# Optimization experiments

Hardware: AMD Instinct MI355X
Metric: run time of the kernel (lower is better)

Reference implementation:

```python
import jax, jax.numpy as jnp
import numpy as np

D_MODEL = 1024
N_HEADS = 16
D_HEAD = D_MODEL // N_HEADS


def setup_inputs() -> dict:
    key = jax.random.key(0)
    k_x, k_wqkv, k_bqkv, k_wo, k_bo = jax.random.split(key, 5)
    B, S = 2, 2048
    x = jax.random.normal(k_x, (B, S, D_MODEL), dtype=jnp.float32)
    # torch Linear: y = x @ W.T + b; store W as [out, in] like torch
    bound1 = 1.0 / np.sqrt(D_MODEL)
    W_qkv = jax.random.uniform(k_wqkv, (3 * D_MODEL, D_MODEL), minval=-bound1, maxval=bound1, dtype=jnp.float32)
    b_qkv = jax.random.uniform(k_bqkv, (3 * D_MODEL,), minval=-bound1, maxval=bound1, dtype=jnp.float32)
    W_out = jax.random.uniform(k_wo, (D_MODEL, D_MODEL), minval=-bound1, maxval=bound1, dtype=jnp.float32)
    b_out = jax.random.uniform(k_bo, (D_MODEL,), minval=-bound1, maxval=bound1, dtype=jnp.float32)
    return {"x": x, "W_qkv": W_qkv, "b_qkv": b_qkv, "W_out": W_out, "b_out": b_out}


def reference(x, W_qkv, b_qkv, W_out, b_out):
    B, S, D = x.shape
    qkv = x @ W_qkv.T + b_qkv                       # [B, S, 3D]
    qkv = qkv.reshape(B, S, 3, N_HEADS, D_HEAD)
    qkv = jnp.transpose(qkv, (2, 0, 3, 1, 4))       # [3, B, H, S, Dh]
    q, k, v = qkv[0], qkv[1], qkv[2]
    scores = jnp.einsum('bhqd,bhkd->bhqk', q, k) / np.sqrt(D_HEAD).astype(np.float32)
    causal = jnp.tril(jnp.ones((S, S), dtype=bool))
    scores = jnp.where(causal[None, None], scores, jnp.float32(-jnp.inf))
    attn = jax.nn.softmax(scores, axis=-1)          # dropout p=0 -> identity
    out = jnp.einsum('bhqk,bhkd->bhqd', attn, v)    # [B, H, S, Dh]
    out = jnp.transpose(out, (0, 2, 1, 3)).reshape(B, S, D)
    return out @ W_out.T + b_out
```

## Files before the change

### kernel.cpp

```cpp
#include <hip/hip_runtime.h>
#include <hip/hip_bf16.h>
#include <cstdint>


#define DEV __device__ __forceinline__

#define VT_STRIDE 2048

using bf16x8 = __attribute__((ext_vector_type(8))) short;
using f32x4  = __attribute__((ext_vector_type(4))) float;

DEV unsigned short f2bf(float f) {
  unsigned u = __builtin_bit_cast(unsigned, f);
  u = (u + 0x7fffu + ((u >> 16) & 1u)) >> 16;
  return (unsigned short)u;
}

typedef __attribute__((address_space(1))) unsigned int as1_uint;
typedef __attribute__((address_space(3))) unsigned int as3_uint;

DEV void gload_lds16(const void* g, void* l) {
  __builtin_amdgcn_global_load_lds(
      (as1_uint*)(uintptr_t)g,
      (as3_uint*)(unsigned int)(uintptr_t)l,
      16, 0, 0);
}

#define N4_X  (4096 * 1024 / 4)
#define N4_WQ (3072 * 1024 / 4)
#define N4_WO (1024 * 1024 / 4)
__global__ __launch_bounds__(256) void cvt_all_k(const float* __restrict__ x,
                                                 const float* __restrict__ wq,
                                                 const float* __restrict__ wo,
                                                 unsigned short* __restrict__ xb,
                                                 unsigned short* __restrict__ wqb,
                                                 unsigned short* __restrict__ wob) {
  int i = blockIdx.x * 256 + threadIdx.x;
  const float* in; unsigned short* out;
  if (i < N4_X)                { in = x;  out = xb; }
  else if (i < N4_X + N4_WQ)   { i -= N4_X;  in = wq; out = wqb; }
  else                         { i -= N4_X + N4_WQ; in = wo; out = wob; }
  float4 v = reinterpret_cast<const float4*>(in)[i];
  ushort4 o;
  o.x = f2bf(v.x); o.y = f2bf(v.y); o.z = f2bf(v.z); o.w = f2bf(v.w);
  reinterpret_cast<ushort4*>(out)[i] = o;
}

__global__ __launch_bounds__(256) void transpose_v_k(const unsigned short* __restrict__ V,
                                                     unsigned short* __restrict__ Vt) {
  const int bh = blockIdx.x;
  const int st = blockIdx.y;
  const int tid = threadIdx.x;
  __shared__ unsigned short T[64 * 64];
  const unsigned short* src = V + ((size_t)bh * 2048 + st * 64) * 64;

#pragma unroll
  for (int it = 0; it < 2; ++it) {
    const int c = it * 256 + tid;
    const int L = c * 16;
    const int S = L ^ (((L >> 10) & 7) << 4);
    gload_lds16((const char*)src + S, (char*)T + L);
  }
  __syncthreads();

#pragma unroll
  for (int it = 0; it < 2; ++it) {
    const int c = it * 256 + tid;
    const int d = c >> 3;
    const int s_off = (c & 7) * 8;
    const int xg = (c & 7) << 4;
    bf16x8 pk;
#pragma unroll
    for (int j = 0; j < 8; ++j)
      pk[j] = *(const short*)((const char*)T + (((s_off + j) * 128 + d * 2) ^ xg));
    *(bf16x8*)(Vt + (size_t)(bh * 64 + d) * VT_STRIDE + st * 64 + s_off) = pk;
  }
}

template <int MODE, int N, int K>
__global__ __launch_bounds__(256) void gemm_bt(const unsigned short* __restrict__ A,
                                               const unsigned short* __restrict__ W,
                                               const float* __restrict__ bias,
                                               float* __restrict__ Cout,
                                               unsigned short* __restrict__ Qp,
                                               unsigned short* __restrict__ Kp,
                                               unsigned short* __restrict__ Vp) {
  __shared__ unsigned short As[128 * 64];
  __shared__ unsigned short Bs[128 * 64];
  const int tid = threadIdx.x;
  const int m0 = blockIdx.x * 128;
  const int n0 = blockIdx.y * 128;
  const int w = tid >> 6, lane = tid & 63, g = lane >> 4, lr = lane & 15;
  const int wr = w >> 1, wc = w & 1;
  const int xr = (lr & 7) << 4;

  f32x4 acc[4][4];
#pragma unroll
  for (int i = 0; i < 4; ++i)
#pragma unroll
    for (int j = 0; j < 4; ++j)
#pragma unroll
      for (int r = 0; r < 4; ++r) acc[i][j][r] = 0.f;

  for (int kt = 0; kt < K; kt += 64) {
#pragma unroll
    for (int it = 0; it < 4; ++it) {
      const int c = it * 256 + tid;
      const int row = c >> 3;
      const int colb = ((c & 7) * 16) ^ ((row & 7) << 4);
      gload_lds16((const char*)(A + (size_t)(m0 + row) * K + kt) + colb, (char*)As + c * 16);
      gload_lds16((const char*)(W + (size_t)(n0 + row) * K + kt) + colb, (char*)Bs + c * 16);
    }
    __syncthreads();
#pragma unroll
    for (int ks = 0; ks < 2; ++ks) {
      bf16x8 af[4], bf[4];
#pragma unroll
      for (int mi = 0; mi < 4; ++mi)
        af[mi] = *(const bf16x8*)((const char*)As +
                   ((((wr * 64 + mi * 16 + lr) * 128) + ks * 64 + g * 16) ^ xr));
#pragma unroll
      for (int ni = 0; ni < 4; ++ni)
        bf[ni] = *(const bf16x8*)((const char*)Bs +
                   ((((wc * 64 + ni * 16 + lr) * 128) + ks * 64 + g * 16) ^ xr));
#pragma unroll
      for (int mi = 0; mi < 4; ++mi)
#pragma unroll
        for (int ni = 0; ni < 4; ++ni)
          acc[mi][ni] = __builtin_amdgcn_mfma_f32_16x16x32_bf16(af[mi], bf[ni], acc[mi][ni], 0, 0, 0);
    }
    __syncthreads();
  }

  if (MODE == 0) {
#pragma unroll
    for (int ni = 0; ni < 4; ++ni) {
      const int col = n0 + wc * 64 + ni * 16 + lr;
      const float bv = bias[col];
#pragma unroll
      for (int mi = 0; mi < 4; ++mi)
#pragma unroll
        for (int r = 0; r < 4; ++r) {
          const int row = m0 + wr * 64 + mi * 16 + g * 4 + r;
          Cout[(size_t)row * N + col] = acc[mi][ni][r] + bv;
        }
    }
  } else {
#pragma unroll
    for (int ni = 0; ni < 4; ++ni) {
      const int col = n0 + wc * 64 + ni * 16 + lr;
      const float bv = bias[col];
      const int which = col >> 10;
      const int h = (col >> 6) & 15;
      const int d = col & 63;
      unsigned short* P = which == 0 ? Qp : which == 1 ? Kp : Vp;
#pragma unroll
      for (int mi = 0; mi < 4; ++mi)
#pragma unroll
        for (int r = 0; r < 4; ++r) {
          const int row = m0 + wr * 64 + mi * 16 + g * 4 + r;
          const int b = row >> 11, s = row & 2047;
          P[(((size_t)(b * 16 + h) * 2048 + s) << 6) + d] = f2bf(acc[mi][ni][r] + bv);
        }
    }
  }
}

__global__ __launch_bounds__(256) void attn_fwd(const unsigned short* __restrict__ Q,
                                                const unsigned short* __restrict__ Kg,
                                                const unsigned short* __restrict__ Vt,
                                                unsigned short* __restrict__ AO) {
  const int bh = blockIdx.x;
  const int qb = blockIdx.y;
  const int tid = threadIdx.x;
  const int w = tid >> 6, lane = tid & 63, g = lane >> 4, lr = lane & 15;
  const unsigned short* Qp = Q  + (size_t)bh * 2048 * 64;
  const unsigned short* Kp = Kg + (size_t)bh * 2048 * 64;
  const unsigned short* Vp = Vt + (size_t)bh * 64 * VT_STRIDE;
  const int b = bh >> 4, h = bh & 15;

  __shared__ unsigned short Ks[2][64 * 64];
  __shared__ unsigned short Vs[2][64 * 64];
  __shared__ unsigned short Pl[4][16 * 64];

  const float C = 0.1803368801f;
  char* Plw = (char*)Pl[w];
  const int xr = (lr & 7) << 4;

  const int L0 = tid * 16,         L1 = (tid + 256) * 16;
  const int G0 = L0 ^ (((L0 >> 7) & 7) << 4);
  const int G1 = L1 ^ (((L1 >> 7) & 7) << 4);

#define STAGE(buf, kvb)                                                                     \
  do {                                                                                      \
    gload_lds16((const char*)Kp + (size_t)(kvb) * 128 + G0, (char*)Ks[buf] + L0);           \
    gload_lds16((const char*)Kp + (size_t)(kvb) * 128 + G1, (char*)Ks[buf] + L1);           \
    gload_lds16((const char*)Vp + (size_t)(G0 >> 7) * (VT_STRIDE * 2) + (size_t)(kvb) * 2 + \
                    (G0 & 127), (char*)Vs[buf] + L0);                                       \
    gload_lds16((const char*)Vp + (size_t)(G1 >> 7) * (VT_STRIDE * 2) + (size_t)(kvb) * 2 + \
                    (G1 & 127), (char*)Vs[buf] + L1);                                       \
  } while (0)

#pragma unroll
  for (int half = 0; half < 2; ++half) {
    const int qt = half ? (31 - qb) : qb;
    const int nb = qt + 1;
    const int qrow0 = qt * 64 + w * 16;

    bf16x8 aq[2];
#pragma unroll
    for (int ks = 0; ks < 2; ++ks)
      aq[ks] = *(const bf16x8*)(Qp + (size_t)(qrow0 + lr) * 64 + ks * 32 + g * 8);

    f32x4 o[4];
    float lp = 0.f;
#pragma unroll
    for (int db = 0; db < 4; ++db)
#pragma unroll
      for (int r = 0; r < 4; ++r) o[db][r] = 0.f;

    STAGE(0, 0);
    int cur = 0;

    for (int t = 0; t < nb; ++t) {
      if (t + 1 < nb) {
        STAGE(cur ^ 1, (t + 1) * 64);
        asm volatile("s_waitcnt vmcnt(4)" ::: "memory");
      } else {
        asm volatile("s_waitcnt vmcnt(0)" ::: "memory");
      }
      __builtin_amdgcn_s_barrier();
      __builtin_amdgcn_sched_barrier(0);

      const char* KsC = (const char*)Ks[cur];
      const char* VsC = (const char*)Vs[cur];

      f32x4 sc[4];
#pragma unroll
      for (int f = 0; f < 4; ++f)
#pragma unroll
        for (int r = 0; r < 4; ++r) sc[f][r] = 0.f;
      __builtin_amdgcn_s_setprio(1);
#pragma unroll
      for (int ks = 0; ks < 2; ++ks)
#pragma unroll
        for (int f = 0; f < 4; ++f) {
          bf16x8 bk = *(const bf16x8*)(KsC + (((f * 16 + lr) * 128 + ks * 64 + g * 16) ^ xr));
          sc[f] = __builtin_amdgcn_mfma_f32_16x16x32_bf16(bk, aq[ks], sc[f], 0, 0, 0);
        }
      __builtin_amdgcn_s_setprio(0);

      if (t == nb - 1) {
        const int thr = w * 16 + lr - g * 4;
#pragma unroll
        for (int f = 0; f < 4; ++f)
#pragma unroll
          for (int r = 0; r < 4; ++r)
            if (f * 16 + r > thr) sc[f][r] = -INFINITY;
      }

#pragma unroll
      for (int f = 0; f < 4; ++f) {
        float p0 = exp2f(sc[f][0] * C);
        float p1 = exp2f(sc[f][1] * C);
        float p2 = exp2f(sc[f][2] * C);
        float p3 = exp2f(sc[f][3] * C);
        sc[f][0] = p0; sc[f][1] = p1; sc[f][2] = p2; sc[f][3] = p3;
        lp += (p0 + p1) + (p2 + p3);
      }

#pragma unroll
      for (int f = 0; f < 4; ++f) {
        unsigned w0, w1;
        asm("v_cvt_pk_bf16_f32 %0, %1, %2" : "=v"(w0) : "v"(sc[f][0]), "v"(sc[f][1]));
        asm("v_cvt_pk_bf16_f32 %0, %1, %2" : "=v"(w1) : "v"(sc[f][2]), "v"(sc[f][3]));
        uint2 pk; pk.x = w0; pk.y = w1;
        *(uint2*)(Plw + ((lr * 128 + f * 32 + g * 8) ^ xr)) = pk;
      }
      asm volatile("s_waitcnt lgkmcnt(0)" ::: "memory");
      __builtin_amdgcn_sched_barrier(0);

      __builtin_amdgcn_s_setprio(1);
#pragma unroll
      for (int ks = 0; ks < 2; ++ks) {
        bf16x8 pa = *(const bf16x8*)(Plw + ((lr * 128 + ks * 64 + g * 16) ^ xr));
#pragma unroll
        for (int db = 0; db < 4; ++db) {
          bf16x8 bv = *(const bf16x8*)(VsC + (((db * 16 + lr) * 128 + ks * 64 + g * 16) ^ xr));
          o[db] = __builtin_amdgcn_mfma_f32_16x16x32_bf16(pa, bv, o[db], 0, 0, 0);
        }
      }
      __builtin_amdgcn_s_setprio(0);

      asm volatile("" ::: "memory");
      __builtin_amdgcn_s_barrier();
      __builtin_amdgcn_sched_barrier(0);
      cur ^= 1;
    }

    lp += __shfl_xor(lp, 16);
    lp += __shfl_xor(lp, 32);
    const float inv = 1.0f / lp;
#pragma unroll
    for (int r = 0; r < 4; ++r) {
      const float linv = __shfl(inv, g * 4 + r);
      const int row = qrow0 + g * 4 + r;
#pragma unroll
      for (int db = 0; db < 4; ++db)
        AO[(size_t)(b * 2048 + row) * 1024 + h * 64 + db * 16 + lr] = f2bf(o[db][r] * linv);
    }
  }
#undef STAGE
}

extern "C" void kernel_launch(void* const* d_in, const int* in_sizes, int n_in,
                              void* d_out, int out_size, void* d_ws, size_t ws_size,
                              hipStream_t stream) {
  const float* x     = (const float*)d_in[0];
  const float* W_qkv = (const float*)d_in[1];
  const float* b_qkv = (const float*)d_in[2];
  const float* W_out = (const float*)d_in[3];
  const float* b_out = (const float*)d_in[4];
  float* out = (float*)d_out;

  char* ws = (char*)d_ws;
  unsigned short* xb  = (unsigned short*)(ws);
  unsigned short* AOb = (unsigned short*)(ws);
  unsigned short* wqb = (unsigned short*)(ws + ((size_t)8 << 20));
  unsigned short* wob = (unsigned short*)(ws + ((size_t)14 << 20));
  unsigned short* Qb  = (unsigned short*)(ws + ((size_t)16 << 20));
  unsigned short* Kb  = (unsigned short*)(ws + ((size_t)24 << 20));
  unsigned short* Vb  = (unsigned short*)(ws + ((size_t)32 << 20));
  unsigned short* Vtb = (unsigned short*)(ws + ((size_t)40 << 20));

  cvt_all_k<<<(N4_X + N4_WQ + N4_WO) / 256, 256, 0, stream>>>(x, W_qkv, W_out, xb, wqb, wob);

  gemm_bt<1, 3072, 1024><<<dim3(32, 24), 256, 0, stream>>>(xb, wqb, b_qkv, nullptr, Qb, Kb, Vb);
  transpose_v_k<<<dim3(32, 32), 256, 0, stream>>>(Vb, Vtb);
  attn_fwd<<<dim3(32, 16), 256, 0, stream>>>(Qb, Kb, Vtb, AOb);
  gemm_bt<0, 1024, 1024><<<dim3(32, 8), 256, 0, stream>>>(AOb, wob, b_out, out, nullptr, nullptr, nullptr);
}
```

Baseline: 124.0 us.

## Double-buffer GEMM LDS tiles to overlap global loads with MFMA

Converts the bf16 GEMM main loop to a two-stage LDS ping-pong: the next K-tile is issued via global_load_lds while the current tile is consumed by MFMAs, with manual vmcnt waits and raw barriers. It also raises wave priority around the MFMA section. This targets exposed global-load latency between K steps, at the cost of doubling LDS use (64KB per block), which may cut occupancy.

```diff
diff --git a/kernel.cpp b/kernel.cpp
--- a/kernel.cpp
+++ b/kernel.cpp
@@ -85,8 +85,8 @@
                                                unsigned short* __restrict__ Qp,
                                                unsigned short* __restrict__ Kp,
                                                unsigned short* __restrict__ Vp) {
-  __shared__ unsigned short As[128 * 64];
-  __shared__ unsigned short Bs[128 * 64];
+  __shared__ unsigned short As[2][128 * 64];
+  __shared__ unsigned short Bs[2][128 * 64];
   const int tid = threadIdx.x;
   const int m0 = blockIdx.x * 128;
   const int n0 = blockIdx.y * 128;
@@ -102,26 +102,46 @@
 #pragma unroll
       for (int r = 0; r < 4; ++r) acc[i][j][r] = 0.f;
 
-  for (int kt = 0; kt < K; kt += 64) {
-#pragma unroll
-    for (int it = 0; it < 4; ++it) {
-      const int c = it * 256 + tid;
-      const int row = c >> 3;
-      const int colb = ((c & 7) * 16) ^ ((row & 7) << 4);
-      gload_lds16((const char*)(A + (size_t)(m0 + row) * K + kt) + colb, (char*)As + c * 16);
-      gload_lds16((const char*)(W + (size_t)(n0 + row) * K + kt) + colb, (char*)Bs + c * 16);
-    }
-    __syncthreads();
+#define GSTAGE(buf, kt)                                                                     \
+  do {                                                                                      \
+    _Pragma("unroll")                                                                       \
+    for (int it = 0; it < 4; ++it) {                                                        \
+      const int c = it * 256 + tid;                                                         \
+      const int row = c >> 3;                                                               \
+      const int colb = ((c & 7) * 16) ^ ((row & 7) << 4);                                   \
+      gload_lds16((const char*)(A + (size_t)(m0 + row) * K + (kt)) + colb,                  \
+                  (char*)As[buf] + c * 16);                                                 \
+      gload_lds16((const char*)(W + (size_t)(n0 + row) * K + (kt)) + colb,                  \
+                  (char*)Bs[buf] + c * 16);                                                 \
+    }                                                                                       \
+  } while (0)
+
+  GSTAGE(0, 0);
+  int cur = 0;
+  const int nsteps = K / 64;
+  for (int step = 0; step < nsteps; ++step) {
+    if (step + 1 < nsteps) {
+      GSTAGE(cur ^ 1, (step + 1) * 64);
+      asm volatile("s_waitcnt vmcnt(8)" ::: "memory");
+    } else {
+      asm volatile("s_waitcnt vmcnt(0)" ::: "memory");
+    }
+    __builtin_amdgcn_s_barrier();
+    __builtin_amdgcn_sched_barrier(0);
+
+    const char* AsC = (const char*)As[cur];
+    const char* BsC = (const char*)Bs[cur];
+    __builtin_amdgcn_s_setprio(1);
 #pragma unroll
     for (int ks = 0; ks < 2; ++ks) {
       bf16x8 af[4], bf[4];
 #pragma unroll
       for (int mi = 0; mi < 4; ++mi)
-        af[mi] = *(const bf16x8*)((const char*)As +
+        af[mi] = *(const bf16x8*)(AsC +
                    ((((wr * 64 + mi * 16 + lr) * 128) + ks * 64 + g * 16) ^ xr));
 #pragma unroll
       for (int ni = 0; ni < 4; ++ni)
-        bf[ni] = *(const bf16x8*)((const char*)Bs +
+        bf[ni] = *(const bf16x8*)(BsC +
                    ((((wc * 64 + ni * 16 + lr) * 128) + ks * 64 + g * 16) ^ xr));
 #pragma unroll
       for (int mi = 0; mi < 4; ++mi)
@@ -129,8 +149,14 @@
         for (int ni = 0; ni < 4; ++ni)
           acc[mi][ni] = __builtin_amdgcn_mfma_f32_16x16x32_bf16(af[mi], bf[ni], acc[mi][ni], 0, 0, 0);
     }
-    __syncthreads();
-  }
+    __builtin_amdgcn_s_setprio(0);
+
+    asm volatile("" ::: "memory");
+    __builtin_amdgcn_s_barrier();
+    __builtin_amdgcn_sched_barrier(0);
+    cur ^= 1;
+  }
+#undef GSTAGE
 
   if (MODE == 0) {
 #pragma unroll
```

Result: faster. 112.7 us (-9.0%).
